# Optimization experiments

Measured on AMD Instinct MI355X. Metric: run time of the kernel, lower is better.

Reference implementation:

```python
import jax, jax.numpy as jnp
import numpy as np

BS = 8; H = 480; W = 640; HFOV = 79.0; CAM_H = 0.88
VR = 100; RES = 5; MAP_CM_LOCAL = 2400; LMAP = 480
MINH = -8; MAXH = 72; NZ = MAXH - MINH            # z bins: int(-40/5)..int(360/5)
GS = RES / 100.0                                   # voxel grid size in meters (0.05)
X1 = MAP_CM_LOCAL // (RES * 2) - VR // 2           # 190
Y1 = MAP_CM_LOCAL // (RES * 2)                     # 240
MIN_Z = int(25 / RES - MINH)                       # 13
MAX_Z = int((CAM_H * 100.0 + 1) / RES - MINH)      # 25
CXp = (W - 1) / 2.0; CZp = (H - 1) / 2.0
FOC = W / 2.0 / np.tan(np.deg2rad(HFOV / 2.0))
NVOX = VR * VR * NZ
N = H * W
EXTRA = 2
DEG = 57.29577951308232
M_LAST = 100000

def setup_inputs() -> dict:
    k = jax.random.key(0); ks = jax.random.split(k, 6)
    rgb = jax.random.uniform(ks[0], (BS, 3, H, W)) * 255.0
    depth = jax.random.uniform(ks[1], (BS, 1, H, W)) * 400.0 + 50.0   # cm, so depth/100 in (0.5, 4.5)
    obs = jnp.concatenate([rgb, depth], axis=1)
    pose_obs = jax.random.normal(ks[2], (BS, 3)) * 0.1
    coords_last = jax.random.randint(ks[3], (M_LAST, 4), 0, BS).astype(jnp.int32)
    feats_last = jax.random.normal(ks[4], (M_LAST, 3 + 3 + EXTRA))
    xy = jax.random.uniform(ks[5], (BS, 2)) * 10.0 + 7.0
    th = jax.random.uniform(jax.random.fold_in(k, 7), (BS, 1)) * 360.0 - 180.0
    poses_last = jnp.concatenate([xy, th], axis=1)
    map_last = (jax.random.uniform(jax.random.fold_in(k, 8), (BS, 4, LMAP, LMAP)) < 0.01).astype(jnp.float32)
    return {"obs": obs, "pose_obs": pose_obs, "coords_last": coords_last,
            "feats_last": feats_last, "poses_last": poses_last, "map_last": map_last}

def _new_pose(pose, rel):
    th = pose[:, 2] / DEG
    y = pose[:, 1] + rel[:, 0] * jnp.sin(th) + rel[:, 1] * jnp.cos(th)
    x = pose[:, 0] + rel[:, 0] * jnp.cos(th) - rel[:, 1] * jnp.sin(th)
    t = pose[:, 2] + rel[:, 2] * DEG
    t = jnp.fmod(t - 180.0, 360.0) + 180.0
    t = jnp.fmod(t + 180.0, 360.0) - 180.0
    return jnp.stack([x, y, t], axis=1)

def _proc(coord, feat, rot, trans, map_i):
    # coord: [N,3] metric points; feat: [N,3] rgb; rot: [3,3]; trans: [3]; map_i: [4,LMAP,LMAP]
    min_c = jnp.array([0.0, 0.0, MINH * GS]); max_c = jnp.array([VR * GS, VR * GS, MAXH * GS])
    valid = jnp.all((coord > min_c) & (coord < max_c), axis=1)
    g = jnp.floor(coord / GS).astype(jnp.int32)                       # voxel grid coords
    vox = (jnp.clip(g[:, 0], 0, VR - 1) * VR + jnp.clip(g[:, 1], 0, VR - 1)) * NZ + jnp.clip(g[:, 2] - MINH, 0, NZ - 1)
    vox = jnp.where(valid, vox, NVOX)                                 # invalid -> dummy voxel
    idx = jnp.arange(N, dtype=jnp.int32)
    first = jax.ops.segment_min(idx, vox, num_segments=NVOX + 1)      # first point per voxel
    is_rep = valid & (first[vox] == idx)                              # voxel-downsample keep mask
    # integer grid-coord path: swap xy, shift, center, rotate, translate, round
    gcf = jnp.stack([g[:, 1] + Y1 - LMAP // 2, g[:, 0] + X1 - LMAP // 2, g[:, 2]], axis=1).astype(jnp.float32)
    gci = jnp.round(gcf @ rot.T + trans).astype(jnp.int32)
    gci = gci.at[:, 2].add(-MINH)
    # metric coord path (same transform scaled by GS)
    cf = jnp.stack([coord[:, 1] + (Y1 - LMAP // 2) * GS, coord[:, 0] + (X1 - LMAP // 2) * GS, coord[:, 2]], axis=1)
    cf = cf @ rot.T + trans * GS
    cf = cf.at[:, 2].add(-MINH * GS)
    # scatter occupancy into local map (get_local_map)
    xs = jnp.clip(gci[:, 0], 0, LMAP - 1); ys = jnp.clip(gci[:, 1], 0, LMAP - 1)
    lm1 = jnp.zeros((LMAP, LMAP)).at[xs, ys].max(is_rep.astype(jnp.float32))
    h_ok = is_rep & (gci[:, 2] >= MIN_Z) & (gci[:, 2] <= MAX_Z)
    lm0 = jnp.zeros((LMAP, LMAP)).at[xs, ys].max(h_ok.astype(jnp.float32))
    z2 = jnp.zeros((LMAP, LMAP))
    out_map = jnp.maximum(jnp.stack([lm0, lm1, z2, z2]), map_i)
    feat_out = jnp.concatenate([cf, feat, jnp.zeros((N, EXTRA))], axis=1) * is_rep[:, None]
    return gci * is_rep[:, None].astype(jnp.int32), feat_out, is_rep, out_map

def reference(obs, pose_obs, coords_last, feats_last, poses_last, map_last):
    current_poses = _new_pose(poses_last, pose_obs)
    st = jnp.stack([current_poses[:, 0] * 100.0 / RES, current_poses[:, 1] * 100.0 / RES, 90.0 - current_poses[:, 2]], axis=1)
    t = st[:, 2] * (np.pi / 180.0)
    c, s = jnp.cos(t), jnp.sin(t)
    zero = jnp.zeros_like(c); one = jnp.ones_like(c)
    rot = jnp.stack([jnp.stack([c, -s, zero], -1), jnp.stack([s, c, zero], -1), jnp.stack([zero, zero, one], -1)], axis=1)
    trans = jnp.stack([st[:, 1], st[:, 0], zero], axis=1)
    # point cloud from depth (du.get_point_cloud_from_z_t, habitat convention)
    depth = obs[:, 3] / 100.0
    u = jnp.arange(W, dtype=jnp.float32); v = jnp.arange(H - 1, -1, -1, dtype=jnp.float32)
    X = (u[None, None, :] - CXp) * depth / FOC + VR * GS / 2.0
    Z = (v[None, :, None] - CZp) * depth / FOC + CAM_H           # + camera height
    coords = jnp.stack([X, depth, Z], axis=-1).reshape(BS, N, 3)
    feats = jnp.transpose(obs[:, :3], (0, 2, 3, 1)).reshape(BS, N, 3)
    gci, feat_out, is_rep, maps = jax.vmap(_proc)(coords, feats, rot, trans, map_last)
    bidx = jnp.broadcast_to(jnp.arange(BS, dtype=jnp.int32)[:, None, None], (BS, N, 1)) * is_rep[:, :, None].astype(jnp.int32)
    new_coords = jnp.concatenate([bidx, gci], axis=2)
    return new_coords, feat_out, maps, current_poses, is_rep
```

## Files before the change

kernel.cpp:

```cpp
#include <hip/hip_runtime.h>
#include <math.h>

#define BSZ 8
#define HH 480
#define WW 640
#define NPIX (HH*WW)
#define VRES 100
#define NZB 80
#define NVOXB (VRES*VRES*NZB)
#define LM 480

#define OFF_COORDS 0LL
#define OFF_FEAT   9830400LL
#define OFF_MAPS   29491200LL
#define OFF_POSES  36864000LL
#define OFF_REP    36864024LL

typedef float fx4 __attribute__((ext_vector_type(4)));

struct PtRes { float depth, X, Z; int g0, g1, g2, vox; bool valid; };

__device__ __forceinline__ int voxid(int c0, int c1, int c2) {
  return (c2 * VRES + c0) * VRES + c1;
}

__device__ __forceinline__ PtRes compute_pt(float draw, int u, int r, float rfoc) {
  PtRes p;
  p.depth = __fmul_rn(draw, 0.01f);
  p.X = __fadd_rn(__fmul_rn(__fmul_rn(__fsub_rn((float)u, 319.5f), p.depth), rfoc), 2.5f);
  p.Z = __fadd_rn(__fmul_rn(__fmul_rn(__fsub_rn((float)(HH - 1 - r), 239.5f), p.depth), rfoc), 0.88f);
  p.valid = (p.X > 0.0f) & (p.X < 5.0f) & (p.depth > 0.0f) & (p.depth < 5.0f)
          & (p.Z > -0.4f) & (p.Z < 3.6f);
  p.g0 = (int)floorf(__fmul_rn(p.X, 20.0f));
  p.g1 = (int)floorf(__fmul_rn(p.depth, 20.0f));
  p.g2 = (int)floorf(__fmul_rn(p.Z, 20.0f));
  int c0 = min(max(p.g0, 0), VRES - 1);
  int c1 = min(max(p.g1, 0), VRES - 1);
  int c2 = min(max(p.g2 + 8, 0), NZB - 1);
  p.vox = voxid(c0, c1, c2);
  return p;
}

__global__ void pose_kernel(const float* __restrict__ pose_obs,
                            const float* __restrict__ poses_last,
                            float* __restrict__ out_poses,
                            float* __restrict__ params) {
  int b = threadIdx.x;
  if (b >= BSZ) return;
  float p0 = poses_last[b*3+0], p1 = poses_last[b*3+1], p2 = poses_last[b*3+2];
  float r0 = pose_obs[b*3+0],  r1 = pose_obs[b*3+1],  r2 = pose_obs[b*3+2];
  const float DEGf = (float)57.29577951308232;
  float thf = __fmul_rn(p2, (float)0.017453292519943295);
  float sth = (float)sin((double)thf);
  float cth = (float)cos((double)thf);
  float y = __fadd_rn(__fadd_rn(p1, __fmul_rn(r0, sth)), __fmul_rn(r1, cth));
  float x = __fsub_rn(__fadd_rn(p0, __fmul_rn(r0, cth)), __fmul_rn(r1, sth));
  float t = __fadd_rn(p2, __fmul_rn(r2, DEGf));
  t = __fadd_rn(fmodf(__fsub_rn(t, 180.0f), 360.0f), 180.0f);
  t = __fsub_rn(fmodf(__fadd_rn(t, 180.0f), 360.0f), 180.0f);
  out_poses[b*3+0] = x; out_poses[b*3+1] = y; out_poses[b*3+2] = t;
  float st0 = __fmul_rn(__fmul_rn(x, 100.0f), 0.2f);
  float st1 = __fmul_rn(__fmul_rn(y, 100.0f), 0.2f);
  float st2 = __fsub_rn(90.0f, t);
  float trad = __fmul_rn(st2, (float)(M_PI / 180.0));
  params[b*4+0] = (float)cos((double)trad);
  params[b*4+1] = (float)sin((double)trad);
  params[b*4+2] = st1;
  params[b*4+3] = st0;
}

#define VPT 8
#define TPB_ROWS (NPIX / VPT)
#define VOXBLK (BSZ * TPB_ROWS / 256)
#define NC (BSZ * 4 * LM * LM / 4)
#define NCBLK (NC / 256)

__global__ __launch_bounds__(256) void vox_store(const float* __restrict__ obs,
                                                 int* __restrict__ first, float rfoc) {
  int b   = blockIdx.x & 7;
  int t   = (blockIdx.x >> 3) * 256 + threadIdx.x;
  int n0 = t * VPT;
  int r = n0 / WW, u0 = n0 % WW;
  const float* rowp = obs + ((size_t)(b*4 + 3) * HH + r) * WW + u0;
  float4 da = *(const float4*)(rowp);
  float4 db = *(const float4*)(rowp + 4);
  float dv[VPT] = {da.x, da.y, da.z, da.w, db.x, db.y, db.z, db.w};
  int* fb = first + b * NVOXB;
  #pragma unroll
  for (int k = 0; k < VPT; ++k) {
    PtRes p = compute_pt(dv[k], u0 + k, r, rfoc);
    if (p.valid) fb[p.vox] = n0 + k;
  }
}

__global__ __launch_bounds__(256) void vox_refine_copy(const float* __restrict__ obs,
                                                       int* __restrict__ first, float rfoc,
                                                       const float* __restrict__ map_last,
                                                       float* __restrict__ out_maps,
                                                       int do_copy) {
  int bid = blockIdx.x;
  if (bid < VOXBLK) {
    int b = bid & 7;
    int t = (bid >> 3) * 256 + threadIdx.x;
    int n0 = t * VPT;
    int r = n0 / WW, u0 = n0 % WW;
    const float* rowp = obs + ((size_t)(b*4 + 3) * HH + r) * WW + u0;
    float4 da = *(const float4*)(rowp);
    float4 db = *(const float4*)(rowp + 4);
    float dv[VPT] = {da.x, da.y, da.z, da.w, db.x, db.y, db.z, db.w};
    int* fb = first + b * NVOXB;
    #pragma unroll
    for (int k = 0; k < VPT; ++k) {
      PtRes p = compute_pt(dv[k], u0 + k, r, rfoc);
      if (p.valid) {
        int n = n0 + k;
        if (n < fb[p.vox]) atomicMin(&fb[p.vox], n);
      }
    }
  } else if (do_copy) {
    int j = (bid - VOXBLK) * 256 + threadIdx.x;
    if (j < NC)
      *(float4*)(out_maps + (size_t)j * 4) = *(const float4*)(map_last + (size_t)j * 4);
  }
}

__global__ __launch_bounds__(256) void fused_kernel(const float* __restrict__ obs,
                                                    const int* __restrict__ first,
                                                    const float* __restrict__ params,
                                                    float* __restrict__ out, float rfoc,
                                                    int write_maps) {
  int b = blockIdx.x & 7;
  int n = (blockIdx.x >> 3) * 256 + threadIdx.x;
  int gid = b * NPIX + n;
  int r = n / WW, u = n % WW;
  float draw = obs[((size_t)(b*4 + 3) * HH + r) * WW + u];
  PtRes p = compute_pt(draw, u, r, rfoc);
  bool rep = p.valid && (first[b * NVOXB + p.vox] == n);

  float c   = params[b*4+0], s = params[b*4+1];
  float tr0 = params[b*4+2], tr1 = params[b*4+3];

  float gcf0 = (float)p.g1, gcf1 = (float)(p.g0 - 50);
  float d0 = fmaf(gcf1, -s, __fmul_rn(gcf0, c));
  float d1 = fmaf(gcf1,  c, __fmul_rn(gcf0, s));
  int gx = (int)rintf(__fadd_rn(d0, tr0));
  int gy = (int)rintf(__fadd_rn(d1, tr1));
  int gz = p.g2 + 8;

  fx4 ncv = rep ? (fx4){(float)b, (float)gx, (float)gy, (float)gz}
                : (fx4){0.f, 0.f, 0.f, 0.f};
  __builtin_nontemporal_store(ncv, (fx4*)(out + OFF_COORDS + (size_t)gid * 4));
  out[OFF_REP + gid] = rep ? 1.0f : 0.0f;

  fx4 f0 = {0.f, 0.f, 0.f, 0.f};
  fx4 f1 = {0.f, 0.f, 0.f, 0.f};
  if (rep) {
    float cf0 = p.depth;
    float cf1 = __fsub_rn(p.X, 2.5f);
    float e0 = __fadd_rn(fmaf(cf1, -s, __fmul_rn(cf0, c)), __fmul_rn(tr0, 0.05f));
    float e1 = __fadd_rn(fmaf(cf1,  c, __fmul_rn(cf0, s)), __fmul_rn(tr1, 0.05f));
    float e2 = __fadd_rn(p.Z, 0.4f);
    float R  = obs[((size_t)(b*4 + 0) * HH + r) * WW + u];
    float G  = obs[((size_t)(b*4 + 1) * HH + r) * WW + u];
    float Bv = obs[((size_t)(b*4 + 2) * HH + r) * WW + u];
    f0 = (fx4){e0, e1, e2, R};
    f1 = (fx4){G, Bv, 0.f, 0.f};
  }
  __builtin_nontemporal_store(f0, (fx4*)(out + OFF_FEAT + (size_t)gid * 8));
  __builtin_nontemporal_store(f1, (fx4*)(out + OFF_FEAT + (size_t)gid * 8 + 4));

  if (write_maps && rep) {
    int xs = min(max(gx, 0), LM - 1);
    int ys = min(max(gy, 0), LM - 1);
    out[OFF_MAPS + ((size_t)(b*4 + 1) * LM + xs) * LM + ys] = 1.0f;
    if (gz >= 13 && gz <= 25)
      out[OFF_MAPS + ((size_t)(b*4 + 0) * LM + xs) * LM + ys] = 1.0f;
  }
}

__global__ __launch_bounds__(256) void copy_maps(const float* __restrict__ map_last,
                                                 float* __restrict__ out_maps) {
  int i = blockIdx.x * blockDim.x + threadIdx.x;
  if (i < NC)
    *(float4*)(out_maps + (size_t)i * 4) = *(const float4*)(map_last + (size_t)i * 4);
}

__global__ __launch_bounds__(256) void scatter_maps(const float* __restrict__ out_coords,
                                                    const float* __restrict__ rep_flags,
                                                    float* __restrict__ out_maps) {
  int gid = blockIdx.x * blockDim.x + threadIdx.x;
  if (gid >= BSZ * NPIX) return;
  if (rep_flags[gid] == 0.0f) return;
  int b = gid / NPIX;
  float4 nc = *(const float4*)(out_coords + (size_t)gid * 4);
  int gx = (int)nc.y, gy = (int)nc.z, gz = (int)nc.w;
  int xs = min(max(gx, 0), LM - 1);
  int ys = min(max(gy, 0), LM - 1);
  out_maps[((size_t)(b*4 + 1) * LM + xs) * LM + ys] = 1.0f;
  if (gz >= 13 && gz <= 25)
    out_maps[((size_t)(b*4 + 0) * LM + xs) * LM + ys] = 1.0f;
}

extern "C" void kernel_launch(void* const* d_in, const int* in_sizes, int n_in,
                              void* d_out, int out_size, void* d_ws, size_t ws_size,
                              hipStream_t stream) {
  const float* obs        = (const float*)d_in[0];
  const float* pose_obs   = (const float*)d_in[1];
  const float* poses_last = (const float*)d_in[4];
  const float* map_last   = (const float*)d_in[5];
  float* out = (float*)d_out;

  const size_t FIRST_BYTES = (size_t)BSZ * NVOXB * sizeof(int);
  bool use_ws = ws_size >= FIRST_BYTES + 4096;
  float* params = (float*)d_ws;
  int*   first  = use_ws ? (int*)((char*)d_ws + 4096) : (int*)(out + OFF_MAPS);

  float focf = (float)((double)WW / 2.0 / tan(39.5 * (M_PI / 180.0)));
  float rfoc = (float)(1.0 / (double)focf);

  hipLaunchKernelGGL(pose_kernel, dim3(1), dim3(64), 0, stream,
                     pose_obs, poses_last, out + OFF_POSES, params);
  hipLaunchKernelGGL(vox_store, dim3(VOXBLK), dim3(256), 0, stream, obs, first, rfoc);
  if (use_ws) {
    hipLaunchKernelGGL(vox_refine_copy, dim3(VOXBLK + NCBLK), dim3(256), 0, stream,
                       obs, first, rfoc, map_last, out + OFF_MAPS, 1);
    hipLaunchKernelGGL(fused_kernel, dim3(BSZ * NPIX / 256), dim3(256), 0, stream,
                       obs, first, params, out, rfoc, 1);
  } else {
    hipLaunchKernelGGL(vox_refine_copy, dim3(VOXBLK), dim3(256), 0, stream,
                       obs, first, rfoc, map_last, out + OFF_MAPS, 0);
    hipLaunchKernelGGL(fused_kernel, dim3(BSZ * NPIX / 256), dim3(256), 0, stream,
                       obs, first, params, out, rfoc, 0);
    hipLaunchKernelGGL(copy_maps, dim3((NC + 255) / 256), dim3(256), 0, stream,
                       map_last, out + OFF_MAPS);
    hipLaunchKernelGGL(scatter_maps, dim3((BSZ * NPIX + 255) / 256), dim3(256), 0, stream,
                       out + OFF_COORDS, out + OFF_REP, out + OFF_MAPS);
  }
}
```

Measured before the change: 122.0 us.

## Fuse pose, voxel store, refine and output into one cooperative kernel

```diff
diff --git a/kernel.cpp b/kernel.cpp
--- a/kernel.cpp
+++ b/kernel.cpp
@@ -1,5 +1,8 @@
 #include <hip/hip_runtime.h>
+#include <hip/hip_cooperative_groups.h>
 #include <math.h>
+
+namespace cg = cooperative_groups;
 
 #define BSZ 8
 #define HH 480
@@ -41,12 +44,9 @@
   return p;
 }
 
-__global__ void pose_kernel(const float* __restrict__ pose_obs,
-                            const float* __restrict__ poses_last,
-                            float* __restrict__ out_poses,
-                            float* __restrict__ params) {
-  int b = threadIdx.x;
-  if (b >= BSZ) return;
+__device__ __forceinline__ void pose_calc(int b, const float* pose_obs,
+                                          const float* poses_last,
+                                          float* out_poses, float* params) {
   float p0 = poses_last[b*3+0], p1 = poses_last[b*3+1], p2 = poses_last[b*3+2];
   float r0 = pose_obs[b*3+0],  r1 = pose_obs[b*3+1],  r2 = pose_obs[b*3+2];
   const float DEGf = (float)57.29577951308232;
@@ -73,7 +73,124 @@
 #define TPB_ROWS (NPIX / VPT)
 #define VOXBLK (BSZ * TPB_ROWS / 256)
 #define NC (BSZ * 4 * LM * LM / 4)
+#define NCB (NC / 8)
 #define NCBLK (NC / 256)
+
+__global__ __launch_bounds__(256, 5) void coop_all(const float* __restrict__ obs,
+                                                   int* __restrict__ first,
+                                                   float* __restrict__ params,
+                                                   float* __restrict__ out, float rfoc,
+                                                   const float* __restrict__ pose_obs,
+                                                   const float* __restrict__ poses_last,
+                                                   const float* __restrict__ map_last) {
+  cg::grid_group grid = cg::this_grid();
+  int b = blockIdx.x & 7;
+  int t = (blockIdx.x >> 3) * 256 + threadIdx.x;
+  int n0 = t * VPT;
+  int r = n0 / WW, u0 = n0 % WW;
+
+  if (blockIdx.x == 0 && threadIdx.x < BSZ)
+    pose_calc(threadIdx.x, pose_obs, poses_last, out + OFF_POSES, params);
+
+  const float* rowp = obs + ((size_t)(b*4 + 3) * HH + r) * WW + u0;
+  float4 da = *(const float4*)(rowp);
+  float4 db = *(const float4*)(rowp + 4);
+  float dv[VPT] = {da.x, da.y, da.z, da.w, db.x, db.y, db.z, db.w};
+  int vox[VPT]; unsigned vmask = 0;
+  int* fb = first + b * NVOXB;
+  #pragma unroll
+  for (int k = 0; k < VPT; ++k) {
+    PtRes p = compute_pt(dv[k], u0 + k, r, rfoc);
+    vox[k] = p.vox;
+    if (p.valid) { vmask |= (1u << k); fb[p.vox] = n0 + k; }
+  }
+  {
+    float* om = out + OFF_MAPS;
+    #pragma unroll
+    for (int it = 0; it < 6; ++it) {
+      int j = b * NCB + t + it * TPB_ROWS;
+      *(float4*)(om + (size_t)j * 4) = *(const float4*)(map_last + (size_t)j * 4);
+    }
+  }
+  __threadfence();
+  grid.sync();
+
+  #pragma unroll
+  for (int k = 0; k < VPT; ++k) {
+    if (vmask & (1u << k)) {
+      int n = n0 + k;
+      if (n < fb[vox[k]]) atomicMin(&fb[vox[k]], n);
+    }
+  }
+  __threadfence();
+  grid.sync();
+
+  float c   = params[b*4+0], s = params[b*4+1];
+  float tr0 = params[b*4+2], tr1 = params[b*4+3];
+  size_t gid0 = (size_t)b * NPIX + n0;
+
+  fx4 repv[2] = {{0.f,0.f,0.f,0.f},{0.f,0.f,0.f,0.f}};
+  #pragma unroll
+  for (int g = 0; g < 2; ++g) {
+    const float* Rp = obs + ((size_t)(b*4 + 0) * HH + r) * WW + u0 + g*4;
+    const float* Gp = obs + ((size_t)(b*4 + 1) * HH + r) * WW + u0 + g*4;
+    const float* Bp = obs + ((size_t)(b*4 + 2) * HH + r) * WW + u0 + g*4;
+    float4 R4 = *(const float4*)(Rp);
+    float4 G4 = *(const float4*)(Gp);
+    float4 B4 = *(const float4*)(Bp);
+    float Rv[4] = {R4.x, R4.y, R4.z, R4.w};
+    float Gv[4] = {G4.x, G4.y, G4.z, G4.w};
+    float Bv4[4] = {B4.x, B4.y, B4.z, B4.w};
+    #pragma unroll
+    for (int q = 0; q < 4; ++q) {
+      int k = g*4 + q;
+      int n = n0 + k;
+      PtRes p = compute_pt(dv[k], u0 + k, r, rfoc);
+      bool rep = ((vmask >> k) & 1u) && (fb[vox[k]] == n);
+
+      float gcf0 = (float)p.g1, gcf1 = (float)(p.g0 - 50);
+      float d0 = fmaf(gcf1, -s, __fmul_rn(gcf0, c));
+      float d1 = fmaf(gcf1,  c, __fmul_rn(gcf0, s));
+      int gx = (int)rintf(__fadd_rn(d0, tr0));
+      int gy = (int)rintf(__fadd_rn(d1, tr1));
+      int gz = p.g2 + 8;
+
+      fx4 ncv = rep ? (fx4){(float)b, (float)gx, (float)gy, (float)gz}
+                    : (fx4){0.f, 0.f, 0.f, 0.f};
+      __builtin_nontemporal_store(ncv, (fx4*)(out + OFF_COORDS + (gid0 + k) * 4));
+
+      fx4 f0 = {0.f,0.f,0.f,0.f}, f1 = {0.f,0.f,0.f,0.f};
+      if (rep) {
+        float cf0 = p.depth;
+        float cf1 = __fsub_rn(p.X, 2.5f);
+        float e0 = __fadd_rn(fmaf(cf1, -s, __fmul_rn(cf0, c)), __fmul_rn(tr0, 0.05f));
+        float e1 = __fadd_rn(fmaf(cf1,  c, __fmul_rn(cf0, s)), __fmul_rn(tr1, 0.05f));
+        float e2 = __fadd_rn(p.Z, 0.4f);
+        f0 = (fx4){e0, e1, e2, Rv[q]};
+        f1 = (fx4){Gv[q], Bv4[q], 0.f, 0.f};
+        repv[g][q] = 1.0f;
+
+        int xs = min(max(gx, 0), LM - 1);
+        int ys = min(max(gy, 0), LM - 1);
+        out[OFF_MAPS + ((size_t)(b*4 + 1) * LM + xs) * LM + ys] = 1.0f;
+        if (gz >= 13 && gz <= 25)
+          out[OFF_MAPS + ((size_t)(b*4 + 0) * LM + xs) * LM + ys] = 1.0f;
+      }
+      __builtin_nontemporal_store(f0, (fx4*)(out + OFF_FEAT + (gid0 + k) * 8));
+      __builtin_nontemporal_store(f1, (fx4*)(out + OFF_FEAT + (gid0 + k) * 8 + 4));
+    }
+  }
+  __builtin_nontemporal_store(repv[0], (fx4*)(out + OFF_REP + gid0));
+  __builtin_nontemporal_store(repv[1], (fx4*)(out + OFF_REP + gid0 + 4));
+}
+
+__global__ void pose_kernel(const float* __restrict__ pose_obs,
+                            const float* __restrict__ poses_last,
+                            float* __restrict__ out_poses,
+                            float* __restrict__ params) {
+  int b = threadIdx.x;
+  if (b < BSZ) pose_calc(b, pose_obs, poses_last, out_poses, params);
+}
 
 __global__ __launch_bounds__(256) void vox_store(const float* __restrict__ obs,
                                                  int* __restrict__ first, float rfoc) {
@@ -218,15 +335,30 @@
   float focf = (float)((double)WW / 2.0 / tan(39.5 * (M_PI / 180.0)));
   float rfoc = (float)(1.0 / (double)focf);
 
-  hipLaunchKernelGGL(pose_kernel, dim3(1), dim3(64), 0, stream,
-                     pose_obs, poses_last, out + OFF_POSES, params);
-  hipLaunchKernelGGL(vox_store, dim3(VOXBLK), dim3(256), 0, stream, obs, first, rfoc);
+  bool coop_ok = false;
   if (use_ws) {
+    int maxB = 0;
+    if (hipOccupancyMaxActiveBlocksPerMultiprocessor(&maxB, coop_all, 256, 0) == hipSuccess)
+      coop_ok = (maxB >= 5);
+  }
+
+  if (coop_ok) {
+    void* args[] = {(void*)&obs, (void*)&first, (void*)&params, (void*)&out,
+                    (void*)&rfoc, (void*)&pose_obs, (void*)&poses_last, (void*)&map_last};
+    hipLaunchCooperativeKernel((const void*)coop_all, dim3(VOXBLK), dim3(256),
+                               args, 0, stream);
+  } else if (use_ws) {
+    hipLaunchKernelGGL(pose_kernel, dim3(1), dim3(64), 0, stream,
+                       pose_obs, poses_last, out + OFF_POSES, params);
+    hipLaunchKernelGGL(vox_store, dim3(VOXBLK), dim3(256), 0, stream, obs, first, rfoc);
     hipLaunchKernelGGL(vox_refine_copy, dim3(VOXBLK + NCBLK), dim3(256), 0, stream,
                        obs, first, rfoc, map_last, out + OFF_MAPS, 1);
     hipLaunchKernelGGL(fused_kernel, dim3(BSZ * NPIX / 256), dim3(256), 0, stream,
                        obs, first, params, out, rfoc, 1);
   } else {
+    hipLaunchKernelGGL(pose_kernel, dim3(1), dim3(64), 0, stream,
+                       pose_obs, poses_last, out + OFF_POSES, params);
+    hipLaunchKernelGGL(vox_store, dim3(VOXBLK), dim3(256), 0, stream, obs, first, rfoc);
     hipLaunchKernelGGL(vox_refine_copy, dim3(VOXBLK), dim3(256), 0, stream,
                        obs, first, rfoc, map_last, out + OFF_MAPS, 0);
     hipLaunchKernelGGL(fused_kernel, dim3(BSZ * NPIX / 256), dim3(256), 0, stream,
```

Result: no change. 121.8 us (-0.2%).
